# Kernel tuning notes

Hardware: AMD Instinct MI355X
Metric: run time of the kernel (lower is better)

## Reference

```python
import jax, jax.numpy as jnp
import numpy as np

M = 128
K = 2 * (M + 1)
EPS = 1e-32
BATCH = 32
D = 20      # latent alphabet size (amino acids)
B_OBS = 20  # observed alphabet size


def _build_transfers(M):
    """Numpy construction of the sparse 0/1 transfer tensors (exact port of
    Profile._make_transfer). Uses slice assignment for the mpp inner loop."""
    K = 2 * (M + 1)
    r0 = np.zeros((M + 1, 3, 2, K), np.float32)
    u0 = np.zeros((M + 1, 3, 2, K), np.float32)
    n0 = np.zeros((K,), np.float32)
    m, g = -1, 0
    for mp in range(M + 1):
        for gp in range(2):
            kp = 2 * mp + 1 - gp
            if m + 1 - g == mp and gp == 0:
                r0[m + 1 - g, g, 0, kp] = 1
                u0[m + 1 - g, g, 0, kp] = 1
            elif m + 1 - g < mp <= M and gp == 0:
                r0[m + 1 - g, g, 0, kp] = 1
                u0[m + 1 - g, g, 1, kp] = 1
                r0[m + 2 - g:mp, 2, 0, kp] = 1
                u0[m + 2 - g:mp, 2, 1, kp] = 1
                r0[mp, 2, 0, kp] = 1
                u0[mp, 2, 0, kp] = 1
            elif m + 1 - g == mp and gp == 1:
                r0[m + 1 - g, g, 1, kp] = 1
            elif m + 1 - g < mp <= M and gp == 1:
                r0[m + 1 - g, g, 0, kp] = 1
                u0[m + 1 - g, g, 1, kp] = 1
                r0[m + 2 - g:mp, 2, 0, kp] = 1
                u0[m + 2 - g:mp, 2, 1, kp] = 1
                r0[mp, 2, 1, kp] = 1
            else:
                n0[kp] = 1
    u0[-1, :, :, :] = 0.0

    rT = np.zeros((M + 1, 3, 2, K, K), np.float32)
    uT = np.zeros((M + 1, 3, 2, K, K), np.float32)
    nT = np.zeros((K, K), np.float32)
    for m in range(M + 1):
        for g in range(2):
            k = 2 * m + 1 - g
            for mp in range(M + 1):
                for gp in range(2):
                    kp = 2 * mp + 1 - gp
                    if m + 1 - g == mp and gp == 0:
                        rT[m + 1 - g, g, 0, k, kp] = 1
                        uT[m + 1 - g, g, 0, k, kp] = 1
                    elif m + 1 - g < mp <= M and gp == 0:
                        rT[m + 1 - g, g, 0, k, kp] = 1
                        uT[m + 1 - g, g, 1, k, kp] = 1
                        rT[m + 2 - g:mp, 2, 0, k, kp] = 1
                        uT[m + 2 - g:mp, 2, 1, k, kp] = 1
                        rT[mp, 2, 0, k, kp] = 1
                        uT[mp, 2, 0, k, kp] = 1
                    elif m + 1 - g == mp and gp == 1:
                        rT[m + 1 - g, g, 1, k, kp] = 1
                    elif m + 1 - g < mp <= M and gp == 1:
                        rT[m + 1 - g, g, 0, k, kp] = 1
                        uT[m + 1 - g, g, 1, k, kp] = 1
                        rT[m + 2 - g:mp, 2, 0, k, kp] = 1
                        uT[m + 2 - g:mp, 2, 1, k, kp] = 1
                        rT[mp, 2, 1, k, kp] = 1
                    elif not (m == M and mp == M and g == 0 and gp == 0):
                        nT[k, kp] = 1
    uT[-1, :, :, :, :] = 0.0

    vx = np.zeros((M + 1, K), np.float32)
    vc = np.zeros((M + 1, K), np.float32)
    for m in range(M + 1):
        vx[m, 2 * m + 1] = 1  # g == 0
        vc[m, 2 * m] = 1      # g == 1
    return r0, u0, n0, rT, uT, nT, vx, vc


def setup_inputs() -> dict:
    key = jax.random.key(0)
    ks = jax.random.split(key, 5)
    ls = jax.nn.log_softmax
    pre = ls(jax.random.normal(ks[0], (BATCH, M + 1, D), jnp.float32), axis=-1)
    ins_seq = ls(jax.random.normal(ks[1], (BATCH, M + 1, D), jnp.float32), axis=-1)
    ins = ls(jax.random.normal(ks[2], (BATCH, M + 1, 3, 2), jnp.float32), axis=-1)
    dele = ls(jax.random.normal(ks[3], (BATCH, M + 1, 3, 2), jnp.float32), axis=-1)
    sub = ls(jax.random.normal(ks[4], (BATCH, D, B_OBS), jnp.float32), axis=-1)
    r0, u0, n0, rT, uT, nT, vx, vc = _build_transfers(M)
    return {
        "precursor_seq_logits": pre,
        "insert_seq_logits": ins_seq,
        "insert_logits": ins,
        "delete_logits": dele,
        "substitute_logits": sub,
        "r_transf_0": jnp.asarray(r0),
        "u_transf_0": jnp.asarray(u0),
        "null_transf_0": jnp.asarray(n0),
        "r_transf": jnp.asarray(rT),
        "u_transf": jnp.asarray(uT),
        "null_transf": jnp.asarray(nT),
        "vx_transf": jnp.asarray(vx),
        "vc_transf": jnp.asarray(vc),
    }


def reference(precursor_seq_logits, insert_seq_logits, insert_logits,
              delete_logits, substitute_logits, r_transf_0, u_transf_0,
              null_transf_0, r_transf, u_transf, null_transf,
              vx_transf, vc_transf):
    neg_inf = -1.0 / EPS  # approximate log(0)
    # initial state distribution over K states
    initial_logits = (jnp.einsum('bijk,ijkl->bl', delete_logits, u_transf_0)
                      + jnp.einsum('bijk,ijkl->bl', insert_logits, r_transf_0)
                      + neg_inf * null_transf_0)
    # KxK transition matrix
    transition_logits = (jnp.einsum('bijk,ijklf->blf', delete_logits, u_transf)
                         + jnp.einsum('bijk,ijklf->blf', insert_logits, r_transf)
                         + neg_inf * null_transf)
    # per-state emission logits over latent alphabet D
    seq_logits = (jnp.einsum('bij,ik->bkj', precursor_seq_logits, vx_transf)
                  + jnp.einsum('bij,ik->bkj', insert_seq_logits, vc_transf))
    # substitution: logsumexp over latent alphabet -> observed alphabet B
    observation_logits = jax.scipy.special.logsumexp(
        seq_logits[..., :, None] + substitute_logits[..., None, :, :], axis=-2)
    return initial_logits, transition_logits, observation_logits
```

## Files before the change

kernel.cpp:

```cpp
#include <hip/hip_runtime.h>

#define MM 128
#define KS 258
#define NSTEP 774
#define NEG_INF_F (-1.0e32f)

#define TRANS_BASE 8256
#define OBS_BASE   2138304

__global__ __launch_bounds__(256) void profile_fused_kernel(
    const float* __restrict__ pre,
    const float* __restrict__ insq,
    const float* __restrict__ ins,
    const float* __restrict__ del,
    const float* __restrict__ sub,
    float* __restrict__ out)
{
    const int b   = blockIdx.y;
    const int chk = blockIdx.x;
    const int tid = threadIdx.x;

    if (chk < 33) {
        __shared__ float2 ps[129];
        __shared__ float  i20[129], i21[129], d20[129];
        __shared__ float  rp[8][6];
        __shared__ int    roff[8];
        __shared__ int    rmeta[8];

        const float* ins_b = ins + b * NSTEP;
        const float* del_b = del + b * NSTEP;

        if (tid < 129) {
            float a0 = ins_b[tid * 6 + 4];
            float d1 = del_b[tid * 6 + 5];
            i20[tid] = a0;
            i21[tid] = ins_b[tid * 6 + 5];
            d20[tid] = del_b[tid * 6 + 4];
            ps[tid]  = make_float2(a0, d1);
        }
        __syncthreads();
        for (int off = 1; off < 129; off <<= 1) {
            float2 add = make_float2(0.f, 0.f);
            if (tid < 129 && tid >= off) add = ps[tid - off];
            __syncthreads();
            if (tid < 129) { float2 v = ps[tid]; v.x += add.x; v.y += add.y; ps[tid] = v; }
            __syncthreads();
        }

        if (tid < 8) {
            int row = chk * 8 + tid;
            if (row <= 258) {
                int a, goff, ooff, special = 0;
                if (row == 258) {
                    a = 0; goff = 0;
                    ooff = b * KS;
                } else {
                    int g = 1 - (row & 1);
                    a = (row >> 1) + (row & 1);
                    int ac = (a <= MM) ? a : MM;
                    goff = ac * 6 + g * 2;
                    ooff = TRANS_BASE + b * (KS * KS) + row * KS;
                    special = (row == 257);
                }
                int ac = (a <= MM) ? a : MM;
                rp[tid][0] = ins_b[goff];
                rp[tid][1] = ins_b[goff + 1];
                rp[tid][2] = del_b[goff];
                rp[tid][3] = del_b[goff + 1];
                rp[tid][4] = ps[ac].x;
                rp[tid][5] = ps[ac].y;
                roff[tid]  = ooff;
                rmeta[tid] = (a << 1) | special;
            } else {
                roff[tid] = -1;
            }
        }
        __syncthreads();

        for (int e = tid; e < 8 * 129; e += 256) {
            int r = e / 129;
            int j = e - r * 129;
            int ooff = roff[r];
            if (ooff < 0) continue;
            int meta = rmeta[r];
            int a    = meta >> 1;
            float ve, vo;
            if (j == a) {
                ve = rp[r][1];
                vo = rp[r][0] + ((a < MM) ? rp[r][2] : 0.0f);
            } else if (j > a) {
                float base = rp[r][0] + rp[r][3]
                           + (ps[j - 1].x - rp[r][4])
                           + (ps[j - 1].y - rp[r][5]);
                ve = base + i21[j];
                vo = base + i20[j] + ((j < MM) ? d20[j] : 0.0f);
            } else {
                ve = NEG_INF_F;
                vo = ((meta & 1) && j == 128) ? 0.0f : NEG_INF_F;
            }
            *(float2*)(out + ooff + 2 * j) = make_float2(ve, vo);
        }
    } else {
        __shared__ float s_sub[400];
        for (int t = tid; t < 400; t += 256) s_sub[t] = sub[b * 400 + t];
        __syncthreads();

        int idx = (chk - 33) * 256 + tid;
        if (idx < KS * 20) {
            int kp = idx / 20;
            int o  = idx - kp * 20;
            int mrow = kp >> 1;
            const float* row = (kp & 1) ? (pre  + (b * (MM + 1) + mrow) * 20)
                                        : (insq + (b * (MM + 1) + mrow) * 20);
            float v[20];
            float mx = -3.0e38f;
#pragma unroll
            for (int j = 0; j < 20; ++j) {
                v[j] = row[j] + s_sub[j * 20 + o];
                mx = fmaxf(mx, v[j]);
            }
            float s = 0.0f;
#pragma unroll
            for (int j = 0; j < 20; ++j) s += expf(v[j] - mx);
            out[OBS_BASE + (b * KS + kp) * 20 + o] = mx + logf(s);
        }
    }
}

extern "C" void kernel_launch(void* const* d_in, const int* in_sizes, int n_in,
                              void* d_out, int out_size, void* d_ws, size_t ws_size,
                              hipStream_t stream) {
    const float* pre  = (const float*)d_in[0];
    const float* insq = (const float*)d_in[1];
    const float* ins  = (const float*)d_in[2];
    const float* del  = (const float*)d_in[3];
    const float* sub  = (const float*)d_in[4];

    hipLaunchKernelGGL(profile_fused_kernel, dim3(54, 32), dim3(256), 0, stream,
                       pre, insq, ins, del, sub, (float*)d_out);
}
```

Measured before the change: 11.60 us.

## Use wavefront shuffle scan and float4 row-flattened stores for transition blocks

Replaces the shared-memory Hillis-Steele prefix scan, which needed many block barriers, with a wavefront __shfl_up scan plus a small cross-wave fixup. Row parameters are packed into float4, and the transition output for each 8-row chunk is written as contiguous float4 stores over the flattened chunk rather than per-row float2 stores. The aim is fewer barriers and wider coalesced writes, at the cost of more index arithmetic per element and a per-element lambda with branching.

```diff
diff --git a/kernel.cpp b/kernel.cpp
--- a/kernel.cpp
+++ b/kernel.cpp
@@ -23,82 +23,112 @@
     if (chk < 33) {
         __shared__ float2 ps[129];
         __shared__ float  i20[129], i21[129], d20[129];
-        __shared__ float  rp[8][6];
-        __shared__ int    roff[8];
-        __shared__ int    rmeta[8];
+        __shared__ float4 rp[9];
+        __shared__ int    rmeta[9];
+        __shared__ float2 s_tot0, s_e128;
 
         const float* ins_b = ins + b * NSTEP;
         const float* del_b = del + b * NSTEP;
 
+        float2 v = make_float2(0.f, 0.f);
         if (tid < 129) {
             float a0 = ins_b[tid * 6 + 4];
             float d1 = del_b[tid * 6 + 5];
             i20[tid] = a0;
             i21[tid] = ins_b[tid * 6 + 5];
             d20[tid] = del_b[tid * 6 + 4];
-            ps[tid]  = make_float2(a0, d1);
-        }
-        __syncthreads();
-        for (int off = 1; off < 129; off <<= 1) {
-            float2 add = make_float2(0.f, 0.f);
-            if (tid < 129 && tid >= off) add = ps[tid - off];
-            __syncthreads();
-            if (tid < 129) { float2 v = ps[tid]; v.x += add.x; v.y += add.y; ps[tid] = v; }
-            __syncthreads();
+            v = make_float2(a0, d1);
         }
 
-        if (tid < 8) {
-            int row = chk * 8 + tid;
-            if (row <= 258) {
-                int a, goff, ooff, special = 0;
-                if (row == 258) {
+        {
+            int nrows = (chk < 32) ? 8 : 3;
+            if (tid < nrows) {
+                int a, goff, special = 0;
+                if (chk == 32 && tid == 2) {
                     a = 0; goff = 0;
-                    ooff = b * KS;
                 } else {
+                    int row = chk * 8 + tid;
                     int g = 1 - (row & 1);
                     a = (row >> 1) + (row & 1);
                     int ac = (a <= MM) ? a : MM;
                     goff = ac * 6 + g * 2;
-                    ooff = TRANS_BASE + b * (KS * KS) + row * KS;
                     special = (row == 257);
                 }
-                int ac = (a <= MM) ? a : MM;
-                rp[tid][0] = ins_b[goff];
-                rp[tid][1] = ins_b[goff + 1];
-                rp[tid][2] = del_b[goff];
-                rp[tid][3] = del_b[goff + 1];
-                rp[tid][4] = ps[ac].x;
-                rp[tid][5] = ps[ac].y;
-                roff[tid]  = ooff;
+                rp[tid] = make_float4(ins_b[goff], ins_b[goff + 1],
+                                      del_b[goff], del_b[goff + 1]);
                 rmeta[tid] = (a << 1) | special;
-            } else {
-                roff[tid] = -1;
             }
+        }
+
+        if (tid < 128) {
+            int lane = tid & 63;
+#pragma unroll
+            for (int d = 1; d < 64; d <<= 1) {
+                float ox = __shfl_up(v.x, d);
+                float oy = __shfl_up(v.y, d);
+                if (lane >= d) { v.x += ox; v.y += oy; }
+            }
+            if (tid == 63) s_tot0 = v;
+        }
+        if (tid == 128) s_e128 = v;
+        __syncthreads();
+        if (tid < 128) {
+            if (tid >= 64) { v.x += s_tot0.x; v.y += s_tot0.y; }
+            ps[tid] = v;
+            if (tid == 127)
+                ps[128] = make_float2(v.x + s_e128.x, v.y + s_e128.y);
         }
         __syncthreads();
 
-        for (int e = tid; e < 8 * 129; e += 256) {
-            int r = e / 129;
-            int j = e - r * 129;
-            int ooff = roff[r];
-            if (ooff < 0) continue;
+        auto entry = [&](int r, int f) -> float {
             int meta = rmeta[r];
             int a    = meta >> 1;
-            float ve, vo;
-            if (j == a) {
-                ve = rp[r][1];
-                vo = rp[r][0] + ((a < MM) ? rp[r][2] : 0.0f);
-            } else if (j > a) {
-                float base = rp[r][0] + rp[r][3]
-                           + (ps[j - 1].x - rp[r][4])
-                           + (ps[j - 1].y - rp[r][5]);
-                ve = base + i21[j];
-                vo = base + i20[j] + ((j < MM) ? d20[j] : 0.0f);
-            } else {
-                ve = NEG_INF_F;
-                vo = ((meta & 1) && j == 128) ? 0.0f : NEG_INF_F;
+            int mp   = f >> 1;
+            int odd  = f & 1;
+            float4 p = rp[r];
+            if (mp == a)
+                return odd ? (p.x + ((a < MM) ? p.z : 0.0f)) : p.y;
+            if (mp > a) {
+                float2 pj = ps[mp - 1], pa = ps[a];
+                float base = p.x + p.w + (pj.x - pa.x) + (pj.y - pa.y);
+                return odd ? (base + i20[mp] + ((mp < MM) ? d20[mp] : 0.0f))
+                           : (base + i21[mp]);
             }
-            *(float2*)(out + ooff + 2 * j) = make_float2(ve, vo);
+            return ((meta & 1) && f == (KS - 1)) ? 0.0f : NEG_INF_F;
+        };
+
+        if (chk < 32) {
+            float* obase = out + TRANS_BASE + b * (KS * KS) + chk * 2064;
+            for (int q = tid; q < 516; q += 256) {
+                int idx = q * 4;
+                int r = idx / KS;
+                int f = idx - r * KS;
+                float v0 = entry(r, f); if (++f == KS) { f = 0; ++r; }
+                float v1 = entry(r, f); if (++f == KS) { f = 0; ++r; }
+                float v2 = entry(r, f); if (++f == KS) { f = 0; ++r; }
+                float v3 = entry(r, f);
+                *(float4*)(obase + idx) = make_float4(v0, v1, v2, v3);
+            }
+        } else {
+            float* obase = out + TRANS_BASE + b * (KS * KS) + 256 * KS;
+            float* ibase = out + b * KS;
+            for (int e = tid; e < 258; e += 256) {
+                if (e < 129) {
+                    int idx = e * 4;
+                    int r = idx / KS;
+                    int f = idx - r * KS;
+                    float v0 = entry(r, f); if (++f == KS) { f = 0; ++r; }
+                    float v1 = entry(r, f); if (++f == KS) { f = 0; ++r; }
+                    float v2 = entry(r, f); if (++f == KS) { f = 0; ++r; }
+                    float v3 = entry(r, f);
+                    *(float4*)(obase + idx) = make_float4(v0, v1, v2, v3);
+                } else {
+                    int j = e - 129;
+                    float ve = entry(2, 2 * j);
+                    float vo = entry(2, 2 * j + 1);
+                    *(float2*)(ibase + 2 * j) = make_float2(ve, vo);
+                }
+            }
         }
     } else {
         __shared__ float s_sub[400];
```

After: 11.60 us. About the same (-0.0%).
